# Kernel optimization log

Measured on AMD Instinct MI355X. Metric: run time of the kernel, lower is better.

## Reference

```python
import jax, jax.numpy as jnp
import numpy as np

B, S, H = 2, 2048, 1024
NH, HD = 16, 64
ROPE_BASE = 10000.0


def setup_inputs() -> dict:
    key = jax.random.key(0)
    ks = jax.random.split(key, 8)
    sc = 1.0 / np.sqrt(H)
    return {
        "hidden_states": jax.random.normal(ks[0], (B, S, H), dtype=jnp.float32),
        "position_ids": jnp.arange(S, dtype=jnp.int64 if jax.config.jax_enable_x64 else jnp.int32)[None, :],
        "Wq": jax.random.normal(ks[1], (H, H), dtype=jnp.float32) * sc,
        "bq": jax.random.normal(ks[2], (H,), dtype=jnp.float32) * 0.02,
        "Wk": jax.random.normal(ks[3], (H, H), dtype=jnp.float32) * sc,
        "bk": jax.random.normal(ks[4], (H,), dtype=jnp.float32) * 0.02,
        "Wv": jax.random.normal(ks[5], (H, H), dtype=jnp.float32) * sc,
        "bv": jax.random.normal(ks[6], (H,), dtype=jnp.float32) * 0.02,
        "Wo": jax.random.normal(ks[7], (H, H), dtype=jnp.float32) * sc,
    }


def _rotate_half(x):
    x1, x2 = x[..., : HD // 2], x[..., HD // 2:]
    return jnp.concatenate((-x2, x1), axis=-1)


def _rope_tables(seq_len, dtype):
    inv_freq = 1.0 / (ROPE_BASE ** (jnp.arange(0, HD, 2, dtype=jnp.float32) / HD))
    t = jnp.arange(seq_len, dtype=jnp.float32)
    freqs = jnp.einsum("s,d->sd", t, inv_freq)          # [S, HD/2]
    emb = jnp.concatenate((freqs, freqs), axis=-1)       # [S, HD]
    return jnp.cos(emb).astype(dtype), jnp.sin(emb).astype(dtype)


def reference(hidden_states, position_ids, Wq, bq, Wk, bk, Wv, bv, Wo):
    bsz, q_len, _ = hidden_states.shape
    # QKV projections (torch Linear: x @ W.T + b)
    q = (hidden_states @ Wq.T + bq).reshape(bsz, q_len, NH, HD).transpose(0, 2, 1, 3)
    k = (hidden_states @ Wk.T + bk).reshape(bsz, q_len, NH, HD).transpose(0, 2, 1, 3)
    v = (hidden_states @ Wv.T + bv).reshape(bsz, q_len, NH, HD).transpose(0, 2, 1, 3)
    # RoPE
    cos, sin = _rope_tables(q_len, hidden_states.dtype)
    cos = cos[position_ids][:, None]  # [1, 1, S, HD] (unsqueeze_dim=1)
    sin = sin[position_ids][:, None]
    q = q * cos + _rotate_half(q) * sin
    k = k * cos + _rotate_half(k) * sin
    # scaled dot-product attention (mask=None, dropout=0)
    scale = 1.0 / jnp.sqrt(jnp.asarray(HD, hidden_states.dtype))
    scores = jnp.einsum("bhqd,bhkd->bhqk", q, k) * scale
    probs = jax.nn.softmax(scores, axis=-1)
    attn = jnp.einsum("bhqk,bhkd->bhqd", probs, v)
    attn = attn.transpose(0, 2, 1, 3).reshape(bsz, q_len, H)
    return attn @ Wo.T
```

## Files before the change

### kernel.cpp

```cpp
#include <hip/hip_runtime.h>
#include <hip/hip_bf16.h>
#include <math.h>

#define SS 2048
#define HH 1024
#define NHH 16
#define HDD 64
#define BH 32
#define MM 4096

typedef unsigned short u16;
using bf16x8 = __attribute__((ext_vector_type(8))) short;
using floatx4 = __attribute__((ext_vector_type(4))) float;

__device__ __forceinline__ u16 f2bf(float f) {
  unsigned u = __float_as_uint(f);
  u += 0x7fffu + ((u >> 16) & 1u);
  return (u16)(u >> 16);
}
__device__ __forceinline__ unsigned pk_bf16(float a, float b) {
  union { __hip_bfloat162 h2; unsigned u; } c;
  c.h2 = __float22bfloat162_rn(float2{a, b});
  return c.u;
}
__device__ __forceinline__ unsigned pk_asm(float a, float b) {
  unsigned r;
  asm("v_cvt_pk_bf16_f32 %0, %1, %2" : "=v"(r) : "v"(a), "v"(b));
  return r;
}
__device__ __forceinline__ void gload_lds16(const u16* g, u16* l) {
  __builtin_amdgcn_global_load_lds(
      (const __attribute__((address_space(1))) void*)g,
      (__attribute__((address_space(3))) void*)l, 16, 0, 0);
}

__global__ __launch_bounds__(256) void convert_bf(
    const float* __restrict__ hs, const float* __restrict__ wq,
    const float* __restrict__ wk, const float* __restrict__ wv,
    const float* __restrict__ wo, const int* __restrict__ pos,
    u16* __restrict__ hs_b, u16* __restrict__ wq_b, u16* __restrict__ wk_b,
    u16* __restrict__ wv_b, u16* __restrict__ wo_b,
    float2* __restrict__ tab) {
  int g = blockIdx.x * 256 + threadIdx.x;
  if (g < 2097152) {
    const float* src;
    u16* dst;
    int off;
    if (g < 1048576) {
      src = hs; dst = hs_b; off = g;
    } else {
      int t = g - 1048576;
      int w = t >> 18;
      off = t & 262143;
      src = (w == 0) ? wq : (w == 1) ? wk : (w == 2) ? wv : wo;
      dst = (w == 0) ? wq_b : (w == 1) ? wk_b : (w == 2) ? wv_b : wo_b;
    }
    float4 v = ((const float4*)src)[off];
    ushort4 o = make_ushort4(f2bf(v.x), f2bf(v.y), f2bf(v.z), f2bf(v.w));
    ((ushort4*)dst)[off] = o;
  } else {
    int idx = g - 2097152;
    int s = idx >> 5, j = idx & 31;
    float p = (float)pos[s];
    const float c0 = 13.287712379549449f / 32.0f;
    float f = p * exp2f(-(float)j * c0);
    float sn, cs;
    sincosf(f, &sn, &cs);
    tab[idx] = float2{cs, sn};
  }
}

__global__ __launch_bounds__(512, 2) void mfma_gemm_qkv(
    const u16* __restrict__ X, const u16* __restrict__ W0,
    const u16* __restrict__ W1, const u16* __restrict__ W2,
    const float* __restrict__ b0, const float* __restrict__ b1,
    const float* __restrict__ b2, const float2* __restrict__ tab,
    u16* __restrict__ O0, u16* __restrict__ O1, u16* __restrict__ O2) {
  __shared__ __align__(16) u16 lds[65536];
  const int tid = threadIdx.x;
  const int lane = tid & 63;
  const int wv = __builtin_amdgcn_readfirstlane(tid >> 6);
  const int l15 = lane & 15, quad = lane >> 4;
  const int sw7 = l15 & 7;
  const int wm = wv >> 2, wn = wv & 3;
  const int r8 = lane >> 3, c7 = lane & 7;

  int wg = blockIdx.x;
  int swz = (wg & 7) * 24 + (wg >> 3);
  int bx = swz % 12, by = swz / 12;
  const int m0 = by * 256;
  const int n0g = bx * 256;
  const int wsel = n0g >> 10;
  const int n0 = n0g & 1023;
  const u16* Wsel = (wsel == 1) ? W1 : (wsel == 2) ? W2 : W0;
  const float* bsel = (wsel == 1) ? b1 : (wsel == 2) ? b2 : b0;
  u16* Osel = (wsel == 1) ? O1 : (wsel == 2) ? O2 : O0;

  u16* const ldsA = lds;
  u16* const ldsB = lds + 32768;

  const int csw = (c7 ^ r8) * 8;
  const int rA0 = (wv >> 2) * 128 + (wv & 3) * 16;
  const int rB0 = (wv >> 1) * 64 + (wv & 1) * 16;
  const u16* gA0a = X + (size_t)(m0 + rA0 + r8) * HH + csw;
  const u16* gA0b = gA0a + 8 * HH;
  const u16* gA2a = gA0a + 64 * HH;
  const u16* gA2b = gA0a + 72 * HH;
  const u16* gB0a = Wsel + (size_t)(n0 + rB0 + r8) * HH + csw;
  const u16* gB0b = gB0a + 8 * HH;
  const u16* gB1a = gB0a + 32 * HH;
  const u16* gB1b = gB0a + 40 * HH;
  const int dA0 = rA0 * 64;
  const int dA2 = dA0 + 4096;
  const int dB0 = rB0 * 64;
  const int dB1 = dB0 + 2048;

#define STAGEU(pa, pb, base, doff, buf)                  \
  do {                                                   \
    u16* d_ = (base) + (buf) * 16384 + (doff);           \
    gload_lds16((pa), d_);                               \
    gload_lds16((pb), d_ + 512);                         \
  } while (0)

  floatx4 acc[8][4];
#pragma unroll
  for (int i = 0; i < 8; ++i)
#pragma unroll
    for (int j = 0; j < 4; ++j) acc[i][j] = (floatx4){0.f, 0.f, 0.f, 0.f};

  STAGEU(gA0a, gA0b, ldsA, dA0, 0);
  STAGEU(gA2a, gA2b, ldsA, dA2, 0);
  STAGEU(gB0a, gB0b, ldsB, dB0, 0);
  STAGEU(gB1a, gB1b, ldsB, dB1, 0);
  STAGEU(gA0a + 64, gA0b + 64, ldsA, dA0, 1);
  STAGEU(gB0a + 64, gB0b + 64, ldsB, dB0, 1);
  STAGEU(gA2a + 64, gA2b + 64, ldsA, dA2, 1);
  asm volatile("s_waitcnt vmcnt(6)" ::: "memory");
  __builtin_amdgcn_s_barrier();

  const u16 *pUB1a = gB1a + 64, *pUB1b = gB1b + 64;
  const u16 *pUA0a = gA0a + 128, *pUA0b = gA0b + 128;
  const u16 *pUB0a = gB0a + 128, *pUB0b = gB0b + 128;
  const u16 *pUA2a = gA2a + 128, *pUA2b = gA2b + 128;

  bf16x8 af[4][2], bf0[2][2], bf1[2][2];

#define LOADA(Ab, hm)                                                     \
  _Pragma("unroll") for (int mb = 0; mb < 4; ++mb) {                      \
    const u16* rp_ = (Ab) + (wm * 128 + (hm) * 64 + mb * 16 + l15) * 64;  \
    af[mb][0] = *(const bf16x8*)&rp_[((quad ^ sw7) * 8)];                 \
    af[mb][1] = *(const bf16x8*)&rp_[(((4 + quad) ^ sw7) * 8)];           \
  }
#define LOADB(dst, Bb, hn)                                                \
  _Pragma("unroll") for (int nq = 0; nq < 2; ++nq) {                      \
    const u16* rp_ = (Bb) + (wn * 64 + (hn) * 32 + nq * 16 + l15) * 64;   \
    dst[nq][0] = *(const bf16x8*)&rp_[((quad ^ sw7) * 8)];                \
    dst[nq][1] = *(const bf16x8*)&rp_[(((4 + quad) ^ sw7) * 8)];          \
  }
#define MFMAQ(bfh, hm, hn)                                                \
  _Pragma("unroll") for (int mb = 0; mb < 4; ++mb)                        \
  _Pragma("unroll") for (int nq = 0; nq < 2; ++nq) {                      \
    acc[(hm) * 4 + mb][(hn) * 2 + nq] =                                   \
        __builtin_amdgcn_mfma_f32_16x16x32_bf16(                          \
            af[mb][0], bfh[nq][0], acc[(hm) * 4 + mb][(hn) * 2 + nq], 0,  \
            0, 0);                                                        \
    acc[(hm) * 4 + mb][(hn) * 2 + nq] =                                   \
        __builtin_amdgcn_mfma_f32_16x16x32_bf16(                          \
            af[mb][1], bfh[nq][1], acc[(hm) * 4 + mb][(hn) * 2 + nq], 0,  \
            0, 0);                                                        \
  }

#pragma unroll 2
  for (int t = 0; t < 16; ++t) {
    const u16* Ac = ldsA + (t & 1) * 16384;
    const u16* Bc = ldsB + (t & 1) * 16384;
    const int nb1 = (t + 1) & 1;
    const int nb2 = t & 1;
    LOADA(Ac, 0);
    LOADB(bf0, Bc, 0);
    if (t < 15) {
      STAGEU(pUB1a, pUB1b, ldsB, dB1, nb1);
      pUB1a += 64; pUB1b += 64;
    }
    __builtin_amdgcn_s_barrier();
    asm volatile("s_waitcnt lgkmcnt(0)" ::: "memory");
    __builtin_amdgcn_s_setprio(1);
    MFMAQ(bf0, 0, 0);
    __builtin_amdgcn_s_setprio(0);
    __builtin_amdgcn_s_barrier();
    LOADB(bf1, Bc, 1);
    if (t < 14) {
      STAGEU(pUA0a, pUA0b, ldsA, dA0, nb2);
      pUA0a += 64; pUA0b += 64;
    }
    __builtin_amdgcn_s_barrier();
    asm volatile("s_waitcnt lgkmcnt(0)" ::: "memory");
    __builtin_amdgcn_s_setprio(1);
    MFMAQ(bf1, 0, 1);
    __builtin_amdgcn_s_setprio(0);
    __builtin_amdgcn_s_barrier();
    LOADA(Ac, 1);
    if (t < 14) {
      STAGEU(pUB0a, pUB0b, ldsB, dB0, nb2);
      pUB0a += 64; pUB0b += 64;
    }
    __builtin_amdgcn_s_barrier();
    asm volatile("s_waitcnt lgkmcnt(0)" ::: "memory");
    __builtin_amdgcn_s_setprio(1);
    MFMAQ(bf0, 1, 0);
    __builtin_amdgcn_s_setprio(0);
    __builtin_amdgcn_s_barrier();
    if (t < 14) {
      STAGEU(pUA2a, pUA2b, ldsA, dA2, nb2);
      pUA2a += 64; pUA2b += 64;
    }
    __builtin_amdgcn_s_setprio(1);
    MFMAQ(bf1, 1, 1);
    __builtin_amdgcn_s_setprio(0);
    if (t < 14) {
      asm volatile("s_waitcnt vmcnt(6)" ::: "memory");
      __builtin_amdgcn_s_barrier();
    } else if (t == 14) {
      asm volatile("s_waitcnt vmcnt(0)" ::: "memory");
      __builtin_amdgcn_s_barrier();
    }
  }
#undef STAGEU
#undef LOADA
#undef LOADB
#undef MFMAQ

  if (wsel < 2) {
    const float qs = (wsel == 0) ? 0.125f * 1.44269504088896f : 1.0f;
    const int colb = n0 + wn * 64;
    const int h = colb >> 6;
    const float bias0 = bsel[colb + l15];
    const float bias1 = bsel[colb + 16 + l15];
    const float bias2 = bsel[colb + 32 + l15];
    const float bias3 = bsel[colb + 48 + l15];
#pragma unroll
    for (int mb = 0; mb < 8; ++mb)
#pragma unroll
      for (int r = 0; r < 4; ++r) {
        int m = m0 + wm * 128 + mb * 16 + quad * 4 + r;
        int b = m >> 11, s = m & (SS - 1);
        float2 t0 = tab[s * 32 + l15];
        float2 t1 = tab[s * 32 + 16 + l15];
        size_t obase = ((size_t)(b * NHH + h) * SS + s) * HDD;
        float x1 = acc[mb][0][r] + bias0;
        float x2 = acc[mb][2][r] + bias2;
        Osel[obase + l15] = f2bf((x1 * t0.x - x2 * t0.y) * qs);
        Osel[obase + 32 + l15] = f2bf((x2 * t0.x + x1 * t0.y) * qs);
        float y1 = acc[mb][1][r] + bias1;
        float y2 = acc[mb][3][r] + bias3;
        Osel[obase + 16 + l15] = f2bf((y1 * t1.x - y2 * t1.y) * qs);
        Osel[obase + 48 + l15] = f2bf((y2 * t1.x + y1 * t1.y) * qs);
      }
  } else {
#pragma unroll
    for (int nb = 0; nb < 4; ++nb) {
      int col = n0 + wn * 64 + nb * 16 + l15;
      int h = col >> 6, d = col & 63;
      float bias = bsel[col];
#pragma unroll
      for (int mb = 0; mb < 8; ++mb) {
        int m = m0 + wm * 128 + mb * 16 + quad * 4;
        int b = m >> 11, s = m & (SS - 1);
        uint2 w2;
        w2.x = pk_bf16(acc[mb][nb][0] + bias, acc[mb][nb][1] + bias);
        w2.y = pk_bf16(acc[mb][nb][2] + bias, acc[mb][nb][3] + bias);
        *(uint2*)&Osel[((size_t)((b * NHH + h) * HDD + d)) * SS + s] = w2;
      }
    }
  }
}

__global__ __launch_bounds__(256) void gemm_out(const u16* __restrict__ X,
                                                const u16* __restrict__ W,
                                                float* __restrict__ Ofp) {
  __shared__ __align__(16) u16 As[2][8192];
  __shared__ __align__(16) u16 Bs[2][8192];
  const int tid = threadIdx.x;
  const int lane = tid & 63;
  const int wv = __builtin_amdgcn_readfirstlane(tid >> 6);
  const int l15 = lane & 15, quad = lane >> 4;
  const int sw7 = l15 & 7;
  const int wm = wv >> 1, wn = wv & 1;
  const int r8 = lane >> 3, c7 = lane & 7;

  int wg = blockIdx.x;
  int swz = (wg & 7) * 32 + (wg >> 3);
  const int n0 = (swz & 7) * 128;
  const int m0 = (swz >> 3) * 128;

  const int csw = (c7 ^ r8) * 8;
  const u16* gA = X + (size_t)(m0 + wv * 32 + r8) * HH + csw;
  const u16* gB = W + (size_t)(n0 + wv * 32 + r8) * HH + csw;
  u16* const dA = &As[0][0] + (wv * 32) * 64;
  u16* const dB = &Bs[0][0] + (wv * 32) * 64;

#define STG_O(tile, buf)                                           \
  _Pragma("unroll") for (int u = 0; u < 4; ++u) {                  \
    gload_lds16(gA + (size_t)u * 8 * HH + (tile) * 64,             \
                dA + (buf) * 8192 + u * 512);                      \
    gload_lds16(gB + (size_t)u * 8 * HH + (tile) * 64,             \
                dB + (buf) * 8192 + u * 512);                      \
  }

  floatx4 acc[4][4];
#pragma unroll
  for (int i = 0; i < 4; ++i)
#pragma unroll
    for (int j = 0; j < 4; ++j) acc[i][j] = (floatx4){0.f, 0.f, 0.f, 0.f};

  STG_O(0, 0);
  STG_O(1, 1);
  asm volatile("s_waitcnt vmcnt(8)" ::: "memory");
  __builtin_amdgcn_s_barrier();

  for (int t = 0; t < 16; ++t) {
    const u16* Ac = &As[0][0] + (t & 1) * 8192;
    const u16* Bc = &Bs[0][0] + (t & 1) * 8192;
    bf16x8 af[4][2], bfr[4][2];
#pragma unroll
    for (int mb = 0; mb < 4; ++mb) {
      const u16* rp = Ac + (wm * 64 + mb * 16 + l15) * 64;
      af[mb][0] = *(const bf16x8*)&rp[(quad ^ sw7) * 8];
      af[mb][1] = *(const bf16x8*)&rp[((4 + quad) ^ sw7) * 8];
    }
#pragma unroll
    for (int nb = 0; nb < 4; ++nb) {
      const u16* rp = Bc + (wn * 64 + nb * 16 + l15) * 64;
      bfr[nb][0] = *(const bf16x8*)&rp[(quad ^ sw7) * 8];
      bfr[nb][1] = *(const bf16x8*)&rp[((4 + quad) ^ sw7) * 8];
    }
    __builtin_amdgcn_s_barrier();
    if (t < 14) STG_O(t + 2, t & 1);
    asm volatile("s_waitcnt lgkmcnt(0)" ::: "memory");
    __builtin_amdgcn_sched_barrier(0);
    __builtin_amdgcn_s_setprio(1);
#pragma unroll
    for (int mb = 0; mb < 4; ++mb)
#pragma unroll
      for (int nb = 0; nb < 4; ++nb) {
        acc[mb][nb] = __builtin_amdgcn_mfma_f32_16x16x32_bf16(
            af[mb][0], bfr[nb][0], acc[mb][nb], 0, 0, 0);
        acc[mb][nb] = __builtin_amdgcn_mfma_f32_16x16x32_bf16(
            af[mb][1], bfr[nb][1], acc[mb][nb], 0, 0, 0);
      }
    __builtin_amdgcn_s_setprio(0);
    if (t < 14) {
      asm volatile("s_waitcnt vmcnt(8)" ::: "memory");
    } else if (t == 14) {
      asm volatile("s_waitcnt vmcnt(0)" ::: "memory");
    }
    __builtin_amdgcn_s_barrier();
  }
#undef STG_O

#pragma unroll
  for (int mb = 0; mb < 4; ++mb)
#pragma unroll
    for (int r = 0; r < 4; ++r) {
      int m = m0 + wm * 64 + mb * 16 + quad * 4 + r;
#pragma unroll
      for (int nb = 0; nb < 4; ++nb)
        Ofp[(size_t)m * HH + n0 + wn * 64 + nb * 16 + l15] = acc[mb][nb][r];
    }
}

__global__ __launch_bounds__(256, 4) void attn_mfma(const u16* __restrict__ Qg,
                                                    const u16* __restrict__ Kg,
                                                    const u16* __restrict__ Vtg,
                                                    u16* __restrict__ A) {
  __shared__ __align__(16) u16 smem[16384];
  u16* const Ks0 = smem;
  u16* const Ks1 = smem + 4096;
  u16* const Vs0 = smem + 8192;
  u16* const Vs1 = smem + 12288;
  float* const lpart = (float*)smem;
  float* const Opart = (float*)smem + 128;

  const int tid = threadIdx.x;
  const int lane = tid & 63;
  const int wv = __builtin_amdgcn_readfirstlane(tid >> 6);
  const int l15 = lane & 15, quad = lane >> 4;
  const int sw7 = l15 & 7;
  const int bh = blockIdx.x, qt = blockIdx.y;
  const size_t hb = (size_t)bh * SS * HDD;
  const int kh = wv >> 1;
  const int qh = wv & 1;

  const int r8 = lane >> 3, c7 = lane & 7;
  const int cs = (c7 ^ r8) * 8;
  const u16* const Kt = Kg + hb;
  const u16* const Vt = Vtg + hb;
  const int row0 = (wv * 2 + 0) * 8 + r8;
  const int row1 = (wv * 2 + 1) * 8 + r8;
  const int koff0 = row0 * HDD + cs;
  const int koff1 = row1 * HDD + cs;
  const int voff0 = row0 * SS + cs;
  const int voff1 = row1 * SS + cs;
  u16* const kd0 = smem + (wv * 2 + 0) * 512;
  u16* const kd1 = smem + (wv * 2 + 1) * 512;

  gload_lds16(Qg + hb + qt * 4096 + koff0, kd0 + 4096);
  gload_lds16(Qg + hb + qt * 4096 + koff1, kd1 + 4096);
  gload_lds16(Kt + koff0, kd0);
  gload_lds16(Kt + koff1, kd1);
  gload_lds16(Vt + voff0, kd0 + 8192);
  gload_lds16(Vt + voff1, kd1 + 8192);
  __syncthreads();

  bf16x8 qf[2][2];
#pragma unroll
  for (int nb = 0; nb < 2; ++nb)
#pragma unroll
    for (int h2 = 0; h2 < 2; ++h2)
      qf[nb][h2] = *(const bf16x8*)&Ks1[(qh * 32 + nb * 16 + l15) * 64 +
                                        (((h2 * 4 + quad) ^ sw7) * 8)];
  __syncthreads();

  float l_acc[2] = {0.f, 0.f};
  floatx4 o[4][2];
#pragma unroll
  for (int dmb = 0; dmb < 4; ++dmb)
#pragma unroll
    for (int nb = 0; nb < 2; ++nb) o[dmb][nb] = (floatx4){0.f, 0.f, 0.f, 0.f};

  auto tile_compute = [&](const u16* ks, const u16* vs) {
    floatx4 st[2][2];
    __builtin_amdgcn_s_setprio(1);
#pragma unroll
    for (int kmb = 0; kmb < 2; ++kmb) {
      int krow = kh * 32 + kmb * 16 + l15;
      bf16x8 ak0 = *(const bf16x8*)&ks[krow * 64 + ((quad ^ sw7) * 8)];
      bf16x8 ak1 = *(const bf16x8*)&ks[krow * 64 + (((4 + quad) ^ sw7) * 8)];
#pragma unroll
      for (int nb = 0; nb < 2; ++nb) {
        floatx4 z = (floatx4){0.f, 0.f, 0.f, 0.f};
        z = __builtin_amdgcn_mfma_f32_16x16x32_bf16(ak0, qf[nb][0], z, 0, 0, 0);
        z = __builtin_amdgcn_mfma_f32_16x16x32_bf16(ak1, qf[nb][1], z, 0, 0, 0);
        st[kmb][nb] = z;
      }
    }
    __builtin_amdgcn_s_setprio(0);

    bf16x8 bp[2];
#pragma unroll
    for (int nb = 0; nb < 2; ++nb) {
      float p00 = __builtin_amdgcn_exp2f(st[0][nb][0]);
      float p01 = __builtin_amdgcn_exp2f(st[0][nb][1]);
      float p02 = __builtin_amdgcn_exp2f(st[0][nb][2]);
      float p03 = __builtin_amdgcn_exp2f(st[0][nb][3]);
      float p10 = __builtin_amdgcn_exp2f(st[1][nb][0]);
      float p11 = __builtin_amdgcn_exp2f(st[1][nb][1]);
      float p12 = __builtin_amdgcn_exp2f(st[1][nb][2]);
      float p13 = __builtin_amdgcn_exp2f(st[1][nb][3]);
      l_acc[nb] += ((p00 + p01) + (p02 + p03)) + ((p10 + p11) + (p12 + p13));
      union { bf16x8 v; unsigned u[4]; } pu;
      pu.u[0] = pk_asm(p00, p01);
      pu.u[1] = pk_asm(p02, p03);
      pu.u[2] = pk_asm(p10, p11);
      pu.u[3] = pk_asm(p12, p13);
      bp[nb] = pu.v;
    }

    const int cb0 = kh * 4 + (quad >> 1);
    const int cb1 = cb0 + 2;
    const int sub = (quad & 1) * 4;
    __builtin_amdgcn_s_setprio(1);
#pragma unroll
    for (int dmb = 0; dmb < 4; ++dmb) {
      int vr = (dmb * 16 + l15) * 64;
      union { bf16x8 v; uint2 d2[2]; } au;
      au.d2[0] = *(const uint2*)&vs[vr + ((cb0 ^ sw7) * 8) + sub];
      au.d2[1] = *(const uint2*)&vs[vr + ((cb1 ^ sw7) * 8) + sub];
#pragma unroll
      for (int nb = 0; nb < 2; ++nb)
        o[dmb][nb] = __builtin_amdgcn_mfma_f32_16x16x32_bf16(au.v, bp[nb],
                                                             o[dmb][nb], 0, 0, 0);
    }
    __builtin_amdgcn_s_setprio(0);
  };

  for (int tt = 0; tt < SS / 64; tt += 2) {
    {
      const int k1 = (tt + 1) * 64 * HDD;
      const int v1 = (tt + 1) * 64;
      gload_lds16(Kt + k1 + koff0, kd0 + 4096);
      gload_lds16(Kt + k1 + koff1, kd1 + 4096);
      gload_lds16(Vt + v1 + voff0, kd0 + 12288);
      gload_lds16(Vt + v1 + voff1, kd1 + 12288);
    }
    tile_compute(Ks0, Vs0);
    __syncthreads();

    if (tt < SS / 64 - 2) {
      const int k2 = (tt + 2) * 64 * HDD;
      const int v2 = (tt + 2) * 64;
      gload_lds16(Kt + k2 + koff0, kd0);
      gload_lds16(Kt + k2 + koff1, kd1);
      gload_lds16(Vt + v2 + voff0, kd0 + 8192);
      gload_lds16(Vt + v2 + voff1, kd1 + 8192);
    }
    tile_compute(Ks1, Vs1);
    __syncthreads();
  }

#pragma unroll
  for (int nb = 0; nb < 2; ++nb) {
    l_acc[nb] += __shfl_xor(l_acc[nb], 16);
    l_acc[nb] += __shfl_xor(l_acc[nb], 32);
  }
  if (quad == 0) {
    lpart[wv * 32 + l15] = l_acc[0];
    lpart[wv * 32 + 16 + l15] = l_acc[1];
  }
  if (kh == 1) {
    float* dst = Opart + qh * (32 * 68);
#pragma unroll
    for (int nb = 0; nb < 2; ++nb)
#pragma unroll
      for (int dmb = 0; dmb < 4; ++dmb)
        *(floatx4*)&dst[(nb * 16 + l15) * 68 + dmb * 16 + quad * 4] =
            o[dmb][nb];
  }
  __syncthreads();
  if (kh == 0) {
    const int b = bh >> 4, h = bh & 15;
    const float* src = Opart + qh * (32 * 68);
    float inv[2];
#pragma unroll
    for (int nb = 0; nb < 2; ++nb)
      inv[nb] = 1.f / (lpart[wv * 32 + nb * 16 + l15] +
                       lpart[(wv + 2) * 32 + nb * 16 + l15]);
#pragma unroll
    for (int nb = 0; nb < 2; ++nb) {
      int s = qt * 64 + qh * 32 + nb * 16 + l15;
#pragma unroll
      for (int dmb = 0; dmb < 4; ++dmb) {
        floatx4 part =
            *(const floatx4*)&src[(nb * 16 + l15) * 68 + dmb * 16 + quad * 4];
        floatx4 tot = (o[dmb][nb] + part) * inv[nb];
        uint2 w2;
        w2.x = pk_asm(tot[0], tot[1]);
        w2.y = pk_asm(tot[2], tot[3]);
        *(uint2*)&A[((size_t)(b * SS + s) * HH) + h * HDD + dmb * 16 +
                    quad * 4] = w2;
      }
    }
  }
}

extern "C" void kernel_launch(void* const* d_in, const int* in_sizes, int n_in,
                              void* d_out, int out_size, void* d_ws,
                              size_t ws_size, hipStream_t stream) {
  const float* hs = (const float*)d_in[0];
  const int* pos = (const int*)d_in[1];
  const float* Wq = (const float*)d_in[2];
  const float* bq = (const float*)d_in[3];
  const float* Wk = (const float*)d_in[4];
  const float* bk = (const float*)d_in[5];
  const float* Wv = (const float*)d_in[6];
  const float* bv = (const float*)d_in[7];
  const float* Wo = (const float*)d_in[8];
  float* out = (float*)d_out;

  u16* hs_b = (u16*)d_ws;
  u16* wq_b = hs_b + 4194304;
  u16* wk_b = wq_b + 1048576;
  u16* wv_b = wk_b + 1048576;
  u16* wo_b = wv_b + 1048576;
  u16* Qb = wo_b + 1048576;
  u16* Kb = Qb + 4194304;
  u16* Vtb = Kb + 4194304;
  u16* Ab = Vtb + 4194304;
  float2* tab = (float2*)(Ab + 4194304);

  hipLaunchKernelGGL(convert_bf, dim3(8448), dim3(256), 0, stream, hs, Wq, Wk,
                     Wv, Wo, pos, hs_b, wq_b, wk_b, wv_b, wo_b, tab);
  hipLaunchKernelGGL(mfma_gemm_qkv, dim3(192), dim3(512), 0, stream, hs_b,
                     wq_b, wk_b, wv_b, bq, bk, bv, tab, Qb, Kb, Vtb);
  hipLaunchKernelGGL(attn_mfma, dim3(32, 32), dim3(256), 0, stream, Qb, Kb,
                     Vtb, Ab);
  hipLaunchKernelGGL(gemm_out, dim3(256), dim3(256), 0, stream, Ab, wo_b,
                     out);
}
```

Before: 180.5 us.

## Triple-buffer K tiles and use partial vmcnt waits in attention loop

The attention kernel now keeps three K buffers and two V buffers in LDS and issues K loads two tiles ahead and V loads one tile ahead. The full __syncthreads after each tile is replaced by s_waitcnt vmcnt(2) plus a raw s_barrier, so the newest prefetch can stay in flight across the barrier. The aim is to hide global-to-LDS latency behind MFMA work. In exchange, LDS use grows from 32 KB to 40 KB per block, which may reduce occupancy under launch_bounds(256,4), and the hand-written waitcnt accounting must stay correct.

```diff
diff --git a/kernel.cpp b/kernel.cpp
--- a/kernel.cpp
+++ b/kernel.cpp
@@ -373,11 +373,7 @@
                                                     const u16* __restrict__ Kg,
                                                     const u16* __restrict__ Vtg,
                                                     u16* __restrict__ A) {
-  __shared__ __align__(16) u16 smem[16384];
-  u16* const Ks0 = smem;
-  u16* const Ks1 = smem + 4096;
-  u16* const Vs0 = smem + 8192;
-  u16* const Vs1 = smem + 12288;
+  __shared__ __align__(16) u16 smem[20480];
   float* const lpart = (float*)smem;
   float* const Opart = (float*)smem + 128;
 
@@ -390,6 +386,14 @@
   const size_t hb = (size_t)bh * SS * HDD;
   const int kh = wv >> 1;
   const int qh = wv & 1;
+
+  u16* const Kb0 = smem;
+  u16* const Kb1 = smem + 4096;
+  u16* const Kb2 = smem + 8192;
+  u16* const Vb0 = smem + 12288;
+  u16* const Vb1 = smem + 16384;
+  u16* Kbuf[3] = {Kb0, Kb1, Kb2};
+  u16* Vbuf[2] = {Vb0, Vb1};
 
   const int r8 = lane >> 3, c7 = lane & 7;
   const int cs = (c7 ^ r8) * 8;
@@ -401,25 +405,38 @@
   const int koff1 = row1 * HDD + cs;
   const int voff0 = row0 * SS + cs;
   const int voff1 = row1 * SS + cs;
-  u16* const kd0 = smem + (wv * 2 + 0) * 512;
-  u16* const kd1 = smem + (wv * 2 + 1) * 512;
-
-  gload_lds16(Qg + hb + qt * 4096 + koff0, kd0 + 4096);
-  gload_lds16(Qg + hb + qt * 4096 + koff1, kd1 + 4096);
-  gload_lds16(Kt + koff0, kd0);
-  gload_lds16(Kt + koff1, kd1);
-  gload_lds16(Vt + voff0, kd0 + 8192);
-  gload_lds16(Vt + voff1, kd1 + 8192);
-  __syncthreads();
+  const int sd0 = (wv * 2 + 0) * 512;
+  const int sd1 = (wv * 2 + 1) * 512;
+
+#define STG_K(tile, bp)                                  \
+  do {                                                   \
+    gload_lds16(Kt + (tile) * 4096 + koff0, (bp) + sd0); \
+    gload_lds16(Kt + (tile) * 4096 + koff1, (bp) + sd1); \
+  } while (0)
+#define STG_V(tile, bp)                                  \
+  do {                                                   \
+    gload_lds16(Vt + (tile) * 64 + voff0, (bp) + sd0);   \
+    gload_lds16(Vt + (tile) * 64 + voff1, (bp) + sd1);   \
+  } while (0)
+
+  gload_lds16(Qg + hb + qt * 4096 + koff0, Kb2 + sd0);
+  gload_lds16(Qg + hb + qt * 4096 + koff1, Kb2 + sd1);
+  STG_K(0, Kb0);
+  STG_V(0, Vb0);
+  STG_K(1, Kb1);
+  asm volatile("s_waitcnt vmcnt(2)" ::: "memory");
+  __builtin_amdgcn_s_barrier();
 
   bf16x8 qf[2][2];
 #pragma unroll
   for (int nb = 0; nb < 2; ++nb)
 #pragma unroll
     for (int h2 = 0; h2 < 2; ++h2)
-      qf[nb][h2] = *(const bf16x8*)&Ks1[(qh * 32 + nb * 16 + l15) * 64 +
+      qf[nb][h2] = *(const bf16x8*)&Kb2[(qh * 32 + nb * 16 + l15) * 64 +
                                         (((h2 * 4 + quad) ^ sw7) * 8)];
-  __syncthreads();
+  asm volatile("s_waitcnt lgkmcnt(0)" ::: "memory");
+  __builtin_amdgcn_sched_barrier(0);
+  __builtin_amdgcn_s_barrier();
 
   float l_acc[2] = {0.f, 0.f};
   floatx4 o[4][2];
@@ -484,35 +501,40 @@
     __builtin_amdgcn_s_setprio(0);
   };
 
-  for (int tt = 0; tt < SS / 64; tt += 2) {
-    {
-      const int k1 = (tt + 1) * 64 * HDD;
-      const int v1 = (tt + 1) * 64;
-      gload_lds16(Kt + k1 + koff0, kd0 + 4096);
-      gload_lds16(Kt + k1 + koff1, kd1 + 4096);
-      gload_lds16(Vt + v1 + voff0, kd0 + 12288);
-      gload_lds16(Vt + v1 + voff1, kd1 + 12288);
-    }
-    tile_compute(Ks0, Vs0);
-    __syncthreads();
-
-    if (tt < SS / 64 - 2) {
-      const int k2 = (tt + 2) * 64 * HDD;
-      const int v2 = (tt + 2) * 64;
-      gload_lds16(Kt + k2 + koff0, kd0);
-      gload_lds16(Kt + k2 + koff1, kd1);
-      gload_lds16(Vt + v2 + voff0, kd0 + 8192);
-      gload_lds16(Vt + v2 + voff1, kd1 + 8192);
-    }
-    tile_compute(Ks1, Vs1);
-    __syncthreads();
-  }
+#define ATILE(t, i)                                                       \
+  do {                                                                    \
+    STG_V((t) + 1, Vbuf[((i) + 1) & 1]);                                  \
+    STG_K((t) + 2, Kbuf[((i) + 2) % 3]);                                  \
+    tile_compute(Kbuf[(i) % 3], Vbuf[(i) & 1]);                           \
+    asm volatile("s_waitcnt vmcnt(2) lgkmcnt(0)" ::: "memory");           \
+    __builtin_amdgcn_sched_barrier(0);                                    \
+    __builtin_amdgcn_s_barrier();                                         \
+  } while (0)
+
+  for (int tb = 0; tb < 30; tb += 6) {
+    ATILE(tb + 0, 0);
+    ATILE(tb + 1, 1);
+    ATILE(tb + 2, 2);
+    ATILE(tb + 3, 3);
+    ATILE(tb + 4, 4);
+    ATILE(tb + 5, 5);
+  }
+  STG_V(31, Vb1);
+  tile_compute(Kb0, Vb0);
+  asm volatile("s_waitcnt vmcnt(0) lgkmcnt(0)" ::: "memory");
+  __builtin_amdgcn_sched_barrier(0);
+  __builtin_amdgcn_s_barrier();
+  tile_compute(Kb1, Vb1);
+#undef ATILE
+#undef STG_K
+#undef STG_V
 
 #pragma unroll
   for (int nb = 0; nb < 2; ++nb) {
     l_acc[nb] += __shfl_xor(l_acc[nb], 16);
     l_acc[nb] += __shfl_xor(l_acc[nb], 32);
   }
+  __syncthreads();
   if (quad == 0) {
     lpart[wv * 32 + l15] = l_acc[0];
     lpart[wv * 32 + 16 + l15] = l_acc[1];
```

Measured after the change: 209.4 us. 1.16x slower.
